# Performance work log

Hardware: AMD Instinct MI355X
Metric: run time of the kernel (lower is better)

## Reference

```python
import jax, jax.numpy as jnp
import numpy as np

B, S, D, H, E, K = 4, 1024, 1024, 4096, 8, 2
CAPACITY_FACTOR = 2.0
T = B * S
CAP = int(T * CAPACITY_FACTOR * K / E)  # 2048


def setup_inputs() -> dict:
    key = jax.random.key(0)
    ks = jax.random.split(key, 6)
    std = 0.02
    return {
        "x": jax.random.normal(ks[0], (B, S, D), dtype=jnp.float32),
        "router_w": jax.random.normal(ks[1], (E, D), dtype=jnp.float32) * std,
        "w1": jax.random.normal(ks[2], (E, D, H), dtype=jnp.float32) * std,
        "b1": jnp.zeros((E, H), dtype=jnp.float32),
        "w2": jax.random.normal(ks[3], (E, H, D), dtype=jnp.float32) * std,
        "b2": jnp.zeros((E, D), dtype=jnp.float32),
    }


def reference(x, router_w, w1, b1, w2, b2):
    # Router (eval mode: no logit noise, no dropout)
    logits = jnp.einsum("bsd,ed->bse", x, router_w)            # [B,S,E]
    probs = jax.nn.softmax(logits, axis=-1)
    topk_p, topk_i = jax.lax.top_k(probs, K)                   # [B,S,K]
    gates = topk_p / jnp.sum(topk_p, axis=-1, keepdims=True)

    xt = x.reshape(T, D)                                        # tokens
    eidx = topk_i.reshape(T * K)                                # expert per slot
    g = gates.reshape(T * K)
    tok = jnp.arange(T * K) // K                                # token id per slot

    # position of each slot within its expert (first-come-first-served capacity)
    oh = jax.nn.one_hot(eidx, E, dtype=jnp.int32)               # [T*K, E]
    pos = jnp.sum((jnp.cumsum(oh, axis=0) - 1) * oh, axis=1)    # [T*K]
    keep = pos < CAP
    pos_c = jnp.where(keep, pos, CAP)                           # overflow -> padding row

    # dispatch: gather tokens into per-expert buffers [E, CAP, D]
    buf = jnp.zeros((E, CAP + 1, D), x.dtype).at[eidx, pos_c].set(xt[tok])
    inp = buf[:, :CAP]

    # per-expert FFN (exact-erf GELU matches torch nn.GELU default)
    h = jax.nn.gelu(jnp.einsum("ecd,edh->ech", inp, w1) + b1[:, None, :],
                    approximate=False)
    out_e = jnp.einsum("ech,eho->eco", h, w2) + b2[:, None, :]  # [E,CAP,D]

    # combine: gather back to slots, weight by gates, sum over k per token
    gathered = out_e[eidx, jnp.minimum(pos_c, CAP - 1)]         # [T*K, D]
    wslot = g * keep.astype(x.dtype)
    out = (gathered * wslot[:, None]).reshape(T, K, D).sum(axis=1).reshape(B, S, D)

    # load-balancing loss
    router_prob_per_expert = probs.mean(axis=(0, 1))            # [E]
    expert_usage = oh.sum(axis=0).astype(x.dtype) / (T * K)
    lb_loss = jnp.sum(router_prob_per_expert * expert_usage) * E
    return out, lb_loss
```

## Files before the change

### kernel.cpp

```cpp
#include <hip/hip_runtime.h>
#include <cstdint>
#include <cstddef>

#define TDIM 4096
#define DDIM 1024
#define HDIM 4096
#define EDIM 8
#define CAPD 2048
#define NSLOT 8192
#define NROUTERBLK 1024

typedef _Float16 f16;
typedef _Float16 f16x2 __attribute__((ext_vector_type(2)));
typedef _Float16 f16x4 __attribute__((ext_vector_type(4)));
typedef _Float16 f16x8 __attribute__((ext_vector_type(8)));
typedef float f32x4 __attribute__((ext_vector_type(4)));

__device__ __forceinline__ void gload16(const void* g, void* l) {
  __builtin_amdgcn_global_load_lds(
      (const __attribute__((address_space(1))) unsigned int*)g,
      (__attribute__((address_space(3))) unsigned int*)l, 16, 0, 0);
}

__device__ __forceinline__ float gelu_fast(float x) {
  float y = 1.5957691216057308f * (x + 0.044715f * x * x * x);
  y = fminf(y, 60.f);
  float e = __expf(y);
  return x * e * __builtin_amdgcn_rcpf(e + 1.f);
}

#define MEMFENCE asm volatile("" ::: "memory")
#define VMCNT(n) asm volatile("s_waitcnt vmcnt(" #n ")" ::: "memory")
#define BAR do { MEMFENCE; __builtin_amdgcn_s_barrier(); MEMFENCE; } while (0)

__global__ __launch_bounds__(256)
void transpose_cvt(const float* __restrict__ src, f16* __restrict__ dst, int R, int C) {
  __shared__ float tile[64][65];
  const int e = blockIdx.z;
  const int c0 = blockIdx.x * 64, r0 = blockIdx.y * 64;
  const int tid = threadIdx.x;
  const float* s = src + (size_t)e * R * C;
  f16* d = dst + (size_t)e * R * C;
  #pragma unroll
  for (int p = 0; p < 4; ++p) {
    const int row = p * 16 + (tid >> 4);
    const int col = (tid & 15) * 4;
    float4 v = *(const float4*)(s + (size_t)(r0 + row) * C + c0 + col);
    tile[row][col] = v.x; tile[row][col + 1] = v.y;
    tile[row][col + 2] = v.z; tile[row][col + 3] = v.w;
  }
  __syncthreads();
  #pragma unroll
  for (int p = 0; p < 4; ++p) {
    const int crow = p * 16 + (tid >> 4);
    const int q = (tid & 15) * 4;
    f16x4 o;
    #pragma unroll
    for (int j = 0; j < 4; ++j) o[j] = (f16)tile[q + j][crow];
    *(f16x4*)(d + (size_t)(c0 + crow) * R + r0 + q) = o;
  }
}

__global__ void router_k(const float* __restrict__ x, const float* __restrict__ rw,
                         int* __restrict__ eidx, float* __restrict__ gates,
                         float* __restrict__ bps) {
  __shared__ float lrw[EDIM * DDIM];
  __shared__ float wps[4][EDIM];
  const int tid = threadIdx.x, lane = tid & 63, wv = tid >> 6;
  for (int i = tid; i < EDIM * DDIM; i += 256) lrw[i] = rw[i];
  __syncthreads();
  const int t = blockIdx.x * 4 + wv;
  float acc[EDIM];
  #pragma unroll
  for (int e = 0; e < EDIM; ++e) acc[e] = 0.f;
  const float* xr = x + (size_t)t * DDIM;
  #pragma unroll
  for (int j = 0; j < DDIM / 64; ++j) {
    float xv = xr[j * 64 + lane];
    #pragma unroll
    for (int e = 0; e < EDIM; ++e) acc[e] += xv * lrw[e * DDIM + j * 64 + lane];
  }
  #pragma unroll
  for (int off = 32; off >= 1; off >>= 1) {
    #pragma unroll
    for (int e = 0; e < EDIM; ++e) acc[e] += __shfl_xor(acc[e], off);
  }
  float mx = acc[0];
  #pragma unroll
  for (int e = 1; e < EDIM; ++e) mx = fmaxf(mx, acc[e]);
  float p[EDIM], s = 0.f;
  #pragma unroll
  for (int e = 0; e < EDIM; ++e) { p[e] = expf(acc[e] - mx); s += p[e]; }
  float inv = 1.f / s;
  #pragma unroll
  for (int e = 0; e < EDIM; ++e) p[e] *= inv;
  int i1 = 0; float p1 = p[0];
  #pragma unroll
  for (int e = 1; e < EDIM; ++e) if (p[e] > p1) { p1 = p[e]; i1 = e; }
  int i2 = (i1 == 0) ? 1 : 0; float p2 = p[i2];
  #pragma unroll
  for (int e = 0; e < EDIM; ++e) if (e != i1 && p[e] > p2) { p2 = p[e]; i2 = e; }
  float gs = 1.f / (p1 + p2);
  if (lane == 0) {
    eidx[2 * t] = i1; eidx[2 * t + 1] = i2;
    gates[2 * t] = p1 * gs; gates[2 * t + 1] = p2 * gs;
    #pragma unroll
    for (int e = 0; e < EDIM; ++e) wps[wv][e] = p[e];
  }
  __syncthreads();
  if (tid < EDIM)
    bps[blockIdx.x * EDIM + tid] = wps[0][tid] + wps[1][tid] + wps[2][tid] + wps[3][tid];
}

__global__ void count_k(const int* __restrict__ eidx, int* __restrict__ cc) {
  __shared__ int h[EDIM];
  const int tid = threadIdx.x;
  if (tid < EDIM) h[tid] = 0;
  __syncthreads();
  atomicAdd(&h[eidx[blockIdx.x * 256 + tid]], 1);
  __syncthreads();
  if (tid < EDIM) cc[blockIdx.x * EDIM + tid] = h[tid];
}

__global__ void scan_k(const int* __restrict__ cc, const float* __restrict__ bps,
                       int* __restrict__ cb, int* __restrict__ counts,
                       int* __restrict__ rowsNeeded, float* __restrict__ lb_out) {
  __shared__ float red[32][EDIM];
  __shared__ int cnt_s[EDIM];
  const int tid = threadIdx.x;
  const int e = tid & 7, g = tid >> 3;
  float s = 0.f;
  for (int j = 0; j < 32; ++j) s += bps[(g + 32 * j) * EDIM + e];
  red[g][e] = s;
  __syncthreads();
  for (int st = 16; st >= 1; st >>= 1) {
    if (g < st) red[g][e] += red[g + st][e];
    __syncthreads();
  }
  if (tid < EDIM) {
    int base = 0;
    for (int c = 0; c < 32; ++c) { cb[c * EDIM + tid] = base; base += cc[c * EDIM + tid]; }
    counts[tid] = base;
    rowsNeeded[tid] = base < CAPD ? base : CAPD;
    cnt_s[tid] = base;
  }
  __syncthreads();
  if (tid == 0) {
    float lb = 0.f;
    for (int ee = 0; ee < EDIM; ++ee)
      lb += (red[0][ee] / (float)TDIM) * ((float)cnt_s[ee] / (float)NSLOT);
    lb_out[0] = lb * (float)EDIM;
  }
}

__global__ void pos_k(const int* __restrict__ eidx, const float* __restrict__ gates,
                      const int* __restrict__ cb, int* __restrict__ posa,
                      float* __restrict__ wslot) {
  __shared__ int wcnt[4][EDIM];
  const int tid = threadIdx.x, lane = tid & 63, wv = tid >> 6;
  const int slot = blockIdx.x * 256 + tid;
  const int e = eidx[slot];
  const unsigned long long below = (1ull << lane) - 1ull;
  int wavepos = 0;
  #pragma unroll
  for (int ee = 0; ee < EDIM; ++ee) {
    unsigned long long m = __ballot(e == ee);
    if (lane == 0) wcnt[wv][ee] = __popcll(m);
    if (e == ee) wavepos = __popcll(m & below);
  }
  __syncthreads();
  int off = 0;
  for (int w = 0; w < wv; ++w) off += wcnt[w][e];
  const int pos = cb[blockIdx.x * EDIM + e] + off + wavepos;
  posa[slot] = pos;
  wslot[slot] = (pos < CAPD) ? gates[slot] : 0.f;
}

__global__ void scatter_k(const float* __restrict__ x, const int* __restrict__ eidx,
                          const int* __restrict__ posa, f16* __restrict__ buf) {
  const int s = blockIdx.x, lane = threadIdx.x;
  const int p = posa[s];
  if (p >= CAPD) return;
  const int e = eidx[s], tok = s >> 1;
  const float4* src = (const float4*)(x + (size_t)tok * DDIM);
  f16x4* dst = (f16x4*)(buf + ((size_t)e * CAPD + p) * DDIM);
  #pragma unroll
  for (int j = 0; j < DDIM / 4 / 64; ++j) {
    float4 v = src[j * 64 + lane];
    f16x4 o; o.x = (f16)v.x; o.y = (f16)v.y; o.z = (f16)v.z; o.w = (f16)v.w;
    dst[j * 64 + lane] = o;
  }
}

#define STAGE(bb, hh2, g) do { \
    const f16* s_ = sP[hh2] + (g) * 64; \
    char* d_ = smem + (bb) * 65536 + (hh2) * 16384 + wv * 1024; \
    gload16(s_, d_); \
    gload16(s_ + (size_t)64 * LD, d_ + 8192); \
  } while (0)

template<int KLEN, int LD, int N, int GELU, int NT, int NKS>
__global__ __launch_bounds__(512, 1)
void gemm256s(const f16* __restrict__ A, const f16* __restrict__ Bt,
              const float* __restrict__ bias, f16* __restrict__ C, size_t pstride,
              const int* __restrict__ rowsNeeded) {
  constexpr int NTT = KLEN / 64;
  __shared__ __align__(128) char smem[131072];
  const int wg = blockIdx.x;
  const int e = wg & 7;
  const int r = wg >> 3;
  const int nt = r % NT;
  const int ks = (r / NT) % NKS;
  const int mt = r / (NT * NKS);
  if (mt * 256 >= rowsNeeded[e]) return;
  const int tid = threadIdx.x, lane = tid & 63, wv = tid >> 6;
  const int wr = wv >> 2, wc = wv & 3;
  const int ro = lane & 15, q4 = (lane >> 4) * 4;
  const int ko0b = (lane >> 4) * 16;
  const f16* aBase = A + ((size_t)e * CAPD + (size_t)mt * 256) * LD + (size_t)ks * KLEN;
  const f16* bBase = Bt + ((size_t)e * N + (size_t)nt * 256) * LD + (size_t)ks * KLEN;
  const int row0 = tid >> 3;
  const int sw0 = ((tid & 7) ^ (row0 & 7)) * 8;

  const f16* sP[4];
  sP[0] = aBase + (size_t)row0 * LD + sw0;
  sP[1] = sP[0] + (size_t)128 * LD;
  sP[2] = bBase + (size_t)row0 * LD + sw0;
  sP[3] = sP[2] + (size_t)128 * LD;

  int aoffs[4][2], boffs[2][2];
  #pragma unroll
  for (int m = 0; m < 4; ++m)
    #pragma unroll
    for (int k = 0; k < 2; ++k) {
      const int rh = m * 16 + ro;
      aoffs[m][k] = wr * 16384 + rh * 128 + ((k * 64 + ko0b) ^ ((rh & 7) << 4));
    }
  #pragma unroll
  for (int n = 0; n < 2; ++n)
    #pragma unroll
    for (int k = 0; k < 2; ++k) {
      const int rh = (wc & 1) * 64 + n * 16 + ro;
      boffs[n][k] = (2 + (wc >> 1)) * 16384 + rh * 128 + ((k * 64 + ko0b) ^ ((rh & 7) << 4));
    }

  f32x4 acc[8][4];
  #pragma unroll
  for (int m = 0; m < 8; ++m)
    #pragma unroll
    for (int n = 0; n < 4; ++n) acc[m][n] = (f32x4){0.f, 0.f, 0.f, 0.f};

  STAGE(0, 0, 0); STAGE(0, 1, 0); STAGE(0, 2, 0); STAGE(0, 3, 0);
  VMCNT(0);
  BAR;

  #pragma unroll 1
  for (int t = 0; t < NTT; ++t) {
    const int cur = t & 1;
    const int cb = cur << 16;
    if (t + 1 < NTT) {
      const int ab = cur ^ 1;
      STAGE(ab, 0, t + 1); STAGE(ab, 1, t + 1);
      STAGE(ab, 2, t + 1); STAGE(ab, 3, t + 1);
    }
    f16x8 af[4][2], bf[4][2];
    #pragma unroll
    for (int n = 0; n < 4; ++n)
      #pragma unroll
      for (int k = 0; k < 2; ++k)
        bf[n][k] = *(const f16x8*)(smem + cb + boffs[n & 1][k] + (n >> 1) * 4096);
    #pragma unroll
    for (int m = 0; m < 4; ++m)
      #pragma unroll
      for (int k = 0; k < 2; ++k)
        af[m][k] = *(const f16x8*)(smem + cb + aoffs[m][k]);
    __builtin_amdgcn_s_setprio(1);
    #pragma unroll
    for (int m = 0; m < 4; ++m)
      #pragma unroll
      for (int n = 0; n < 4; ++n)
        #pragma unroll
        for (int k = 0; k < 2; ++k)
          acc[m][n] = __builtin_amdgcn_mfma_f32_16x16x32_f16(af[m][k], bf[n][k], acc[m][n], 0, 0, 0);
    __builtin_amdgcn_s_setprio(0);
    #pragma unroll
    for (int m = 0; m < 4; ++m)
      #pragma unroll
      for (int k = 0; k < 2; ++k)
        af[m][k] = *(const f16x8*)(smem + cb + aoffs[m][k] + 8192);
    __builtin_amdgcn_s_setprio(1);
    #pragma unroll
    for (int m = 0; m < 4; ++m)
      #pragma unroll
      for (int n = 0; n < 4; ++n)
        #pragma unroll
        for (int k = 0; k < 2; ++k)
          acc[4 + m][n] = __builtin_amdgcn_mfma_f32_16x16x32_f16(af[m][k], bf[n][k], acc[4 + m][n], 0, 0, 0);
    __builtin_amdgcn_s_setprio(0);
    if (t + 1 < NTT) VMCNT(0);
    BAR;
  }

  float bv[4];
  #pragma unroll
  for (int n = 0; n < 4; ++n)
    bv[n] = (ks == 0) ? bias[e * N + nt * 256 + wc * 64 + n * 16 + ro] : 0.f;
  f16* Ct = (f16*)(smem + wv * 16384);
  #pragma unroll
  for (int m = 0; m < 8; ++m)
    #pragma unroll
    for (int n = 0; n < 4; ++n)
      #pragma unroll
      for (int i = 0; i < 4; ++i) {
        const int row = m * 16 + q4 + i;
        float v = acc[m][n][i] + bv[n];
        if (GELU) v = gelu_fast(v);
        *(f16*)((char*)Ct + row * 128 + ((((n * 16 + ro) * 2)) ^ (((row >> 2) & 3) << 5))) = (f16)v;
      }
  asm volatile("s_waitcnt lgkmcnt(0)" ::: "memory");
  f16* Cp = C + (size_t)ks * pstride;
  const size_t crow0 = (size_t)e * CAPD + mt * 256 + wr * 128;
  const int ccol0 = nt * 256 + wc * 64;
  #pragma unroll
  for (int j = 0; j < 16; ++j) {
    const int idx = j * 64 + lane;
    const int rr = idx >> 3, c2 = (idx & 7) * 16;
    f16x8 v = *(const f16x8*)((const char*)Ct + rr * 128 + (c2 ^ (((rr >> 2) & 3) << 5)));
    *(f16x8*)(Cp + (crow0 + rr) * N + ccol0 + (idx & 7) * 8) = v;
  }
}

__global__ void combine_k(const f16* __restrict__ pA, const f16* __restrict__ pB,
                          const int* __restrict__ eidx, const int* __restrict__ posa,
                          const float* __restrict__ wslot, float* __restrict__ out) {
  const int t = blockIdx.x, tid = threadIdx.x;
  const int s0 = 2 * t, s1 = 2 * t + 1;
  const int e0 = eidx[s0], e1 = eidx[s1];
  int p0 = posa[s0]; p0 = p0 < CAPD - 1 ? p0 : CAPD - 1;
  int p1 = posa[s1]; p1 = p1 < CAPD - 1 ? p1 : CAPD - 1;
  const float g0 = wslot[s0], g1 = wslot[s1];
  const size_t o0 = ((size_t)e0 * CAPD + p0) * DDIM;
  const size_t o1 = ((size_t)e1 * CAPD + p1) * DDIM;
  const f16x2* r0a = (const f16x2*)(pA + o0);
  const f16x2* r0b = (const f16x2*)(pB + o0);
  const f16x2* r1a = (const f16x2*)(pA + o1);
  const f16x2* r1b = (const f16x2*)(pB + o1);
  float2* o = (float2*)(out + (size_t)t * DDIM);
  #pragma unroll
  for (int j = tid; j < DDIM / 2; j += 256) {
    f16x2 a0 = r0a[j], a1 = r0b[j], b0 = r1a[j], b1 = r1b[j];
    o[j] = make_float2(
        g0 * ((float)a0.x + (float)a1.x) + g1 * ((float)b0.x + (float)b1.x),
        g0 * ((float)a0.y + (float)a1.y) + g1 * ((float)b0.y + (float)b1.y));
  }
}

extern "C" void kernel_launch(void* const* d_in, const int* in_sizes, int n_in,
                              void* d_out, int out_size, void* d_ws, size_t ws_size,
                              hipStream_t stream) {
  (void)in_sizes; (void)n_in; (void)out_size; (void)ws_size;
  const float* x  = (const float*)d_in[0];
  const float* rw = (const float*)d_in[1];
  const float* w1 = (const float*)d_in[2];
  const float* b1 = (const float*)d_in[3];
  const float* w2 = (const float*)d_in[4];
  const float* b2 = (const float*)d_in[5];
  float* out = (float*)d_out;

  char* ws = (char*)d_ws;
  size_t off = 0;
  auto alloc = [&](size_t b) { void* p = ws + off; off += (b + 255) & ~(size_t)255; return p; };
  f16* w1t   = (f16*)alloc((size_t)EDIM * DDIM * HDIM * 2);
  f16* w2t   = (f16*)alloc((size_t)EDIM * DDIM * HDIM * 2);
  f16* buf   = (f16*)alloc((size_t)EDIM * CAPD * DDIM * 2);
  f16* hbuf  = (f16*)alloc((size_t)EDIM * CAPD * HDIM * 2);
  const size_t PSTRIDE = (size_t)EDIM * CAPD * DDIM;
  f16* outeA = (f16*)alloc(PSTRIDE * 2);
  f16* outeB = (f16*)alloc(PSTRIDE * 2);
  int*   eidx   = (int*)alloc(NSLOT * 4);
  int*   posa   = (int*)alloc(NSLOT * 4);
  float* gatesA = (float*)alloc(NSLOT * 4);
  float* wslotA = (float*)alloc(NSLOT * 4);
  int*   cc     = (int*)alloc(32 * EDIM * 4);
  int*   cb     = (int*)alloc(32 * EDIM * 4);
  int*   counts = (int*)alloc(EDIM * 4);
  int*   rowsN  = (int*)alloc(EDIM * 4);
  float* bps    = (float*)alloc(NROUTERBLK * EDIM * 4);
  (void)outeB;

  transpose_cvt<<<dim3(HDIM / 64, DDIM / 64, EDIM), 256, 0, stream>>>(w1, w1t, DDIM, HDIM);
  transpose_cvt<<<dim3(DDIM / 64, HDIM / 64, EDIM), 256, 0, stream>>>(w2, w2t, HDIM, DDIM);

  router_k<<<NROUTERBLK, 256, 0, stream>>>(x, rw, eidx, gatesA, bps);
  count_k<<<32, 256, 0, stream>>>(eidx, cc);
  scan_k<<<1, 256, 0, stream>>>(cc, bps, cb, counts, rowsN, out + (size_t)TDIM * DDIM);
  pos_k<<<32, 256, 0, stream>>>(eidx, gatesA, cb, posa, wslotA);
  scatter_k<<<NSLOT, 64, 0, stream>>>(x, eidx, posa, buf);

  gemm256s<DDIM, DDIM, HDIM, 1, 16, 1><<<1024, 512, 0, stream>>>(
      buf, w1t, b1, hbuf, 0, rowsN);

  gemm256s<HDIM / 2, HDIM, DDIM, 0, 4, 2><<<512, 512, 0, stream>>>(
      hbuf, w2t, b2, outeA, PSTRIDE, rowsN);

  combine_k<<<TDIM, 256, 0, stream>>>(outeA, outeA + PSTRIDE, eidx, posa, wslotA, out);
}
```

Before: 339.5 us.

## Replace 256x256 expert GEMM tiles with 128x128 tiles at two blocks per CU

Shrinks the expert FFN GEMM tile from 256x256 with 512 threads and 128KB of LDS to 128x128 with 256 threads and 64KB of LDS, with launch bounds asking for two resident blocks per CU. Grid sizes grow four-fold so the capacity-skip logic works at finer granularity, and the second GEMM still uses a split-K of two. The aim is more concurrent workgroups to hide latency and better load balance over uneven expert row counts. In exchange, arithmetic intensity per tile falls and global and LDS traffic per FLOP rises, and the setprio hints are dropped.

```diff
diff --git a/kernel.cpp b/kernel.cpp
--- a/kernel.cpp
+++ b/kernel.cpp
@@ -30,8 +30,6 @@
 }
 
 #define MEMFENCE asm volatile("" ::: "memory")
-#define VMCNT(n) asm volatile("s_waitcnt vmcnt(" #n ")" ::: "memory")
-#define BAR do { MEMFENCE; __builtin_amdgcn_s_barrier(); MEMFENCE; } while (0)
 
 __global__ __launch_bounds__(256)
 void transpose_cvt(const float* __restrict__ src, f16* __restrict__ dst, int R, int C) {
@@ -192,122 +190,100 @@
   }
 }
 
-#define STAGE(bb, hh2, g) do { \
-    const f16* s_ = sP[hh2] + (g) * 64; \
-    char* d_ = smem + (bb) * 65536 + (hh2) * 16384 + wv * 1024; \
+#define STAGE(bb, hh, g) do { \
+    const f16* s_ = sP[hh] + (g) * 64; \
+    char* d_ = smem + (bb) * 32768 + (hh) * 8192 + wv * 1024; \
     gload16(s_, d_); \
-    gload16(s_ + (size_t)64 * LD, d_ + 8192); \
+    gload16(s_ + (size_t)32 * LD, d_ + 4096); \
   } while (0)
 
 template<int KLEN, int LD, int N, int GELU, int NT, int NKS>
-__global__ __launch_bounds__(512, 1)
-void gemm256s(const f16* __restrict__ A, const f16* __restrict__ Bt,
-              const float* __restrict__ bias, f16* __restrict__ C, size_t pstride,
-              const int* __restrict__ rowsNeeded) {
+__global__ __launch_bounds__(256, 2)
+void gemm128(const f16* __restrict__ A, const f16* __restrict__ Bt,
+             const float* __restrict__ bias, f16* __restrict__ C, size_t pstride,
+             const int* __restrict__ rowsNeeded) {
   constexpr int NTT = KLEN / 64;
-  __shared__ __align__(128) char smem[131072];
+  __shared__ __align__(128) char smem[65536];
   const int wg = blockIdx.x;
   const int e = wg & 7;
   const int r = wg >> 3;
   const int nt = r % NT;
   const int ks = (r / NT) % NKS;
   const int mt = r / (NT * NKS);
-  if (mt * 256 >= rowsNeeded[e]) return;
+  if (mt * 128 >= rowsNeeded[e]) return;
   const int tid = threadIdx.x, lane = tid & 63, wv = tid >> 6;
-  const int wr = wv >> 2, wc = wv & 3;
+  const int wr = wv >> 1, wc = wv & 1;
   const int ro = lane & 15, q4 = (lane >> 4) * 4;
   const int ko0b = (lane >> 4) * 16;
-  const f16* aBase = A + ((size_t)e * CAPD + (size_t)mt * 256) * LD + (size_t)ks * KLEN;
-  const f16* bBase = Bt + ((size_t)e * N + (size_t)nt * 256) * LD + (size_t)ks * KLEN;
+  const f16* aBase = A + ((size_t)e * CAPD + (size_t)mt * 128) * LD + (size_t)ks * KLEN;
+  const f16* bBase = Bt + ((size_t)e * N + (size_t)nt * 128) * LD + (size_t)ks * KLEN;
   const int row0 = tid >> 3;
   const int sw0 = ((tid & 7) ^ (row0 & 7)) * 8;
 
   const f16* sP[4];
   sP[0] = aBase + (size_t)row0 * LD + sw0;
-  sP[1] = sP[0] + (size_t)128 * LD;
+  sP[1] = sP[0] + (size_t)64 * LD;
   sP[2] = bBase + (size_t)row0 * LD + sw0;
-  sP[3] = sP[2] + (size_t)128 * LD;
-
-  int aoffs[4][2], boffs[2][2];
+  sP[3] = sP[2] + (size_t)64 * LD;
+
+  int aoffs[4][2], boffs[4][2];
   #pragma unroll
   for (int m = 0; m < 4; ++m)
     #pragma unroll
     for (int k = 0; k < 2; ++k) {
-      const int rh = m * 16 + ro;
-      aoffs[m][k] = wr * 16384 + rh * 128 + ((k * 64 + ko0b) ^ ((rh & 7) << 4));
+      const int rh = wr * 64 + m * 16 + ro;
+      aoffs[m][k] = rh * 128 + ((k * 64 + ko0b) ^ ((rh & 7) << 4));
+      const int rb = wc * 64 + m * 16 + ro;
+      boffs[m][k] = 16384 + rb * 128 + ((k * 64 + ko0b) ^ ((rb & 7) << 4));
     }
-  #pragma unroll
-  for (int n = 0; n < 2; ++n)
-    #pragma unroll
-    for (int k = 0; k < 2; ++k) {
-      const int rh = (wc & 1) * 64 + n * 16 + ro;
-      boffs[n][k] = (2 + (wc >> 1)) * 16384 + rh * 128 + ((k * 64 + ko0b) ^ ((rh & 7) << 4));
-    }
-
-  f32x4 acc[8][4];
-  #pragma unroll
-  for (int m = 0; m < 8; ++m)
+
+  f32x4 acc[4][4];
+  #pragma unroll
+  for (int m = 0; m < 4; ++m)
     #pragma unroll
     for (int n = 0; n < 4; ++n) acc[m][n] = (f32x4){0.f, 0.f, 0.f, 0.f};
 
   STAGE(0, 0, 0); STAGE(0, 1, 0); STAGE(0, 2, 0); STAGE(0, 3, 0);
-  VMCNT(0);
-  BAR;
+  asm volatile("s_waitcnt vmcnt(0)" ::: "memory");
+  __builtin_amdgcn_sched_barrier(0);
+  __builtin_amdgcn_s_barrier(); MEMFENCE;
 
   #pragma unroll 1
   for (int t = 0; t < NTT; ++t) {
-    const int cur = t & 1;
-    const int cb = cur << 16;
+    const int cb = (t & 1) << 15;
     if (t + 1 < NTT) {
-      const int ab = cur ^ 1;
+      const int ab = (t & 1) ^ 1;
       STAGE(ab, 0, t + 1); STAGE(ab, 1, t + 1);
       STAGE(ab, 2, t + 1); STAGE(ab, 3, t + 1);
     }
     f16x8 af[4][2], bf[4][2];
     #pragma unroll
-    for (int n = 0; n < 4; ++n)
-      #pragma unroll
-      for (int k = 0; k < 2; ++k)
-        bf[n][k] = *(const f16x8*)(smem + cb + boffs[n & 1][k] + (n >> 1) * 4096);
-    #pragma unroll
     for (int m = 0; m < 4; ++m)
       #pragma unroll
-      for (int k = 0; k < 2; ++k)
+      for (int k = 0; k < 2; ++k) {
         af[m][k] = *(const f16x8*)(smem + cb + aoffs[m][k]);
-    __builtin_amdgcn_s_setprio(1);
-    #pragma unroll
-    for (int m = 0; m < 4; ++m)
+        bf[m][k] = *(const f16x8*)(smem + cb + boffs[m][k]);
+      }
+    #pragma unroll
+    for (int k = 0; k < 2; ++k)
       #pragma unroll
-      for (int n = 0; n < 4; ++n)
+      for (int m = 0; m < 4; ++m)
         #pragma unroll
-        for (int k = 0; k < 2; ++k)
+        for (int n = 0; n < 4; ++n)
           acc[m][n] = __builtin_amdgcn_mfma_f32_16x16x32_f16(af[m][k], bf[n][k], acc[m][n], 0, 0, 0);
-    __builtin_amdgcn_s_setprio(0);
-    #pragma unroll
-    for (int m = 0; m < 4; ++m)
-      #pragma unroll
-      for (int k = 0; k < 2; ++k)
-        af[m][k] = *(const f16x8*)(smem + cb + aoffs[m][k] + 8192);
-    __builtin_amdgcn_s_setprio(1);
-    #pragma unroll
-    for (int m = 0; m < 4; ++m)
-      #pragma unroll
-      for (int n = 0; n < 4; ++n)
-        #pragma unroll
-        for (int k = 0; k < 2; ++k)
-          acc[4 + m][n] = __builtin_amdgcn_mfma_f32_16x16x32_f16(af[m][k], bf[n][k], acc[4 + m][n], 0, 0, 0);
-    __builtin_amdgcn_s_setprio(0);
-    if (t + 1 < NTT) VMCNT(0);
-    BAR;
+    asm volatile("s_waitcnt lgkmcnt(0)" ::: "memory");
+    asm volatile("s_waitcnt vmcnt(0)" ::: "memory");
+    __builtin_amdgcn_sched_barrier(0);
+    __builtin_amdgcn_s_barrier(); MEMFENCE;
   }
 
   float bv[4];
   #pragma unroll
   for (int n = 0; n < 4; ++n)
-    bv[n] = (ks == 0) ? bias[e * N + nt * 256 + wc * 64 + n * 16 + ro] : 0.f;
-  f16* Ct = (f16*)(smem + wv * 16384);
-  #pragma unroll
-  for (int m = 0; m < 8; ++m)
+    bv[n] = (ks == 0) ? bias[e * N + nt * 128 + wc * 64 + n * 16 + ro] : 0.f;
+  f16* Ct = (f16*)(smem + wv * 8192);
+  #pragma unroll
+  for (int m = 0; m < 4; ++m)
     #pragma unroll
     for (int n = 0; n < 4; ++n)
       #pragma unroll
@@ -315,14 +291,15 @@
         const int row = m * 16 + q4 + i;
         float v = acc[m][n][i] + bv[n];
         if (GELU) v = gelu_fast(v);
-        *(f16*)((char*)Ct + row * 128 + ((((n * 16 + ro) * 2)) ^ (((row >> 2) & 3) << 5))) = (f16)v;
+        *(f16*)((char*)Ct + row * 128 + (((n * 16 + ro) * 2) ^ (((row >> 2) & 3) << 5))) = (f16)v;
       }
   asm volatile("s_waitcnt lgkmcnt(0)" ::: "memory");
+  __builtin_amdgcn_sched_barrier(0);
   f16* Cp = C + (size_t)ks * pstride;
-  const size_t crow0 = (size_t)e * CAPD + mt * 256 + wr * 128;
-  const int ccol0 = nt * 256 + wc * 64;
-  #pragma unroll
-  for (int j = 0; j < 16; ++j) {
+  const size_t crow0 = (size_t)e * CAPD + mt * 128 + wr * 64;
+  const int ccol0 = nt * 128 + wc * 64;
+  #pragma unroll
+  for (int j = 0; j < 8; ++j) {
     const int idx = j * 64 + lane;
     const int rr = idx >> 3, c2 = (idx & 7) * 16;
     f16x8 v = *(const f16x8*)((const char*)Ct + rr * 128 + (c2 ^ (((rr >> 2) & 3) << 5)));
@@ -397,10 +374,10 @@
   pos_k<<<32, 256, 0, stream>>>(eidx, gatesA, cb, posa, wslotA);
   scatter_k<<<NSLOT, 64, 0, stream>>>(x, eidx, posa, buf);
 
-  gemm256s<DDIM, DDIM, HDIM, 1, 16, 1><<<1024, 512, 0, stream>>>(
+  gemm128<DDIM, DDIM, HDIM, 1, 32, 1><<<4096, 256, 0, stream>>>(
       buf, w1t, b1, hbuf, 0, rowsN);
 
-  gemm256s<HDIM / 2, HDIM, DDIM, 0, 4, 2><<<512, 512, 0, stream>>>(
+  gemm128<HDIM / 2, HDIM, DDIM, 0, 8, 2><<<2048, 256, 0, stream>>>(
       hbuf, w2t, b2, outeA, PSTRIDE, rowsN);
 
   combine_k<<<TDIM, 256, 0, stream>>>(outeA, outeA + PSTRIDE, eidx, posa, wslotA, out);
```

After: 318.5 us. 6.2% less time.
